# Optimization experiments

Hardware: AMD Instinct MI355X
Metric: run time of the kernel (lower is better)

Reference implementation:

```python
import jax, jax.numpy as jnp
import numpy as np

NUM_HEADS = 4
NUM_GROUPS = 8
EPS = 1e-5


def group_norm(x, gamma, beta):
    B, C, H, W = x.shape
    xg = x.reshape(B, NUM_GROUPS, C // NUM_GROUPS, H, W)
    mean = xg.mean(axis=(2, 3, 4), keepdims=True)
    var = xg.var(axis=(2, 3, 4), keepdims=True)
    xn = ((xg - mean) * jax.lax.rsqrt(var + EPS)).reshape(B, C, H, W)
    return xn * gamma[None, :, None, None] + beta[None, :, None, None]


def setup_inputs() -> dict:
    key = jax.random.key(0)
    k1, k2, k3 = jax.random.split(key, 3)
    B, C, H, W = 16, 512, 32, 32
    x = jax.random.normal(k1, (B, C, H, W), dtype=jnp.float32)
    gn_gamma = jnp.ones((C,), dtype=jnp.float32)
    gn_beta = jnp.zeros((C,), dtype=jnp.float32)
    w_qkv = jax.random.normal(k2, (3 * C, C), dtype=jnp.float32) * 0.02
    w_proj = jax.random.normal(k3, (C, C), dtype=jnp.float32) * 0.02
    b_proj = jnp.zeros((C,), dtype=jnp.float32)
    return {"x": x, "gn_gamma": gn_gamma, "gn_beta": gn_beta,
            "w_qkv": w_qkv, "w_proj": w_proj, "b_proj": b_proj}


def reference(x, gn_gamma, gn_beta, w_qkv, w_proj, b_proj):
    B, C, H, W = x.shape
    nh = NUM_HEADS
    hd = C // nh
    N = H * W

    x_norm = group_norm(x, gn_gamma, gn_beta)
    # 1x1 conv == channel matmul: (B,C,H,W) x (3C,C) -> (B,3C,H,W)
    qkv = jnp.einsum('bchw,dc->bdhw', x_norm, w_qkv)
    qkv = qkv.reshape(B, 3, nh, hd, N)
    q, k, v = qkv[:, 0], qkv[:, 1], qkv[:, 2]  # each (B, nh, hd, N)

    scale = hd ** (-0.5)
    attn = jnp.einsum('bhci,bhcj->bhij', q, k) * scale  # (B, nh, N, N)
    attn = jax.nn.softmax(attn, axis=-1)
    out = jnp.einsum('bhij,bhcj->bhci', attn, v)  # (B, nh, hd, N)
    out = out.reshape(B, C, H, W)

    proj = jnp.einsum('bchw,dc->bdhw', out, w_proj) + b_proj[None, :, None, None]
    return x + proj
```

## Files before the change

### kernel.cpp

```cpp
#include <hip/hip_runtime.h>
#include <stdint.h>

typedef unsigned char u8;
typedef unsigned short u16;
typedef unsigned int u32;
typedef long long i64;
typedef __attribute__((ext_vector_type(8))) short short8;
typedef __attribute__((ext_vector_type(4))) float f32x4;
typedef __attribute__((ext_vector_type(16))) float f32x16;
typedef __attribute__((ext_vector_type(4))) u32 u32x4;

#define BATCH 16
#define CCH   512
#define NPIX  1024
#define NGRP  8
#define CPG   64
#define NHEAD 4
#define HDIM  128

__device__ __forceinline__ u16 f2bf(float f) {
  union { float f; u32 u; } v; v.f = f;
  u32 u = v.u;
  u32 r = (u + 0x7FFFu + ((u >> 16) & 1u)) >> 16;
  return (u16)r;
}
__device__ __forceinline__ u8 f2fp8(float f) {
  return (u8)(__builtin_amdgcn_cvt_pk_fp8_f32(f, 0.f, 0, false) & 0xff);
}
__device__ __forceinline__ u32 pack4_fp8(float a, float b, float c, float d) {
  u32 w = (u32)__builtin_amdgcn_cvt_pk_fp8_f32(a, b, 0, false);
  w = (u32)__builtin_amdgcn_cvt_pk_fp8_f32(c, d, (int)w, true);
  return w;
}

__device__ __forceinline__ void gload16(const void* g, void* l) {
  typedef __attribute__((address_space(3))) u32 L;
  typedef __attribute__((address_space(1))) const u32 G;
  __builtin_amdgcn_global_load_lds((G*)(uintptr_t)g, (L*)(u32)(uintptr_t)l, 16, 0, 0);
}

#define PLSWAP(a, b) asm("v_permlane32_swap_b32 %0, %1" : "+v"(a), "+v"(b))

__device__ __forceinline__ short8 rd512(const char* base, int r, int ck, int hi) {
  int byte = ((r >> 2) * 512) +
             ((((r & 3) * 128) + ck * 32 + hi * 16) ^ (((r >> 2) & 15) << 4));
  return *reinterpret_cast<const short8*>(base + byte);
}

__global__ void gn_stats_k(const float* __restrict__ x, float* __restrict__ part) {
  int bg = blockIdx.x >> 3, sl = blockIdx.x & 7;
  const float* p = x + (size_t)bg * (CPG * NPIX) + sl * 8192;
  float s = 0.f, ss = 0.f;
  for (int i = threadIdx.x; i < 2048; i += 256) {
    float4 v = reinterpret_cast<const float4*>(p)[i];
    s  += v.x + v.y + v.z + v.w;
    ss += v.x*v.x + v.y*v.y + v.z*v.z + v.w*v.w;
  }
  for (int o = 32; o > 0; o >>= 1) { s += __shfl_down(s, o); ss += __shfl_down(ss, o); }
  __shared__ float sh[8];
  int wid = threadIdx.x >> 6;
  if ((threadIdx.x & 63) == 0) { sh[wid*2] = s; sh[wid*2+1] = ss; }
  __syncthreads();
  if (threadIdx.x == 0) {
    part[blockIdx.x*2]   = sh[0]+sh[2]+sh[4]+sh[6];
    part[blockIdx.x*2+1] = sh[1]+sh[3]+sh[5]+sh[7];
  }
}

__global__ __launch_bounds__(256) void gn_apply_t(const float* __restrict__ x,
                                                  const float* __restrict__ gamma,
                                                  const float* __restrict__ beta,
                                                  const float* __restrict__ part,
                                                  u16* __restrict__ xnT) {
  const int p0 = blockIdx.x * 64;
  const int c0 = blockIdx.y * 64;
  const int b  = blockIdx.z;
  __shared__ float lt[64][66];

  const int bg = b * NGRP + (c0 >> 6);
  float s = 0.f, ss = 0.f;
  #pragma unroll
  for (int k2 = 0; k2 < 8; ++k2) { s += part[(bg*8 + k2)*2]; ss += part[(bg*8 + k2)*2 + 1]; }
  const float invn = 1.f / (float)(CPG * NPIX);
  const float mean = s * invn;
  const float rstd = rsqrtf(ss * invn - mean * mean + 1e-5f);

  const int t = threadIdx.x;
  #pragma unroll
  for (int pass = 0; pass < 4; ++pass) {
    int c   = c0 + (t >> 4) + pass * 16;
    int pix = p0 + (t & 15) * 4;
    float ga = gamma[c] * rstd;
    float be = beta[c] - mean * ga;
    float4 v = *reinterpret_cast<const float4*>(&x[((size_t)(b*CCH + c)) * NPIX + pix]);
    int pl = (t & 15) * 4, cl = (t >> 4) + pass * 16;
    lt[pl+0][cl] = v.x*ga + be;
    lt[pl+1][cl] = v.y*ga + be;
    lt[pl+2][cl] = v.z*ga + be;
    lt[pl+3][cl] = v.w*ga + be;
  }
  __syncthreads();
  const int pl = t >> 2, cq = (t & 3) * 16;
  u32 wbuf[8];
  #pragma unroll
  for (int e = 0; e < 8; ++e) {
    u16 lo = f2bf(lt[pl][cq + e*2]);
    u16 hi = f2bf(lt[pl][cq + e*2 + 1]);
    wbuf[e] = (u32)lo | ((u32)hi << 16);
  }
  u32* dst = (u32*)&xnT[((size_t)(b*NPIX + p0 + pl)) * CCH + c0 + cq];
  #pragma unroll
  for (int e = 0; e < 8; ++e) dst[e] = wbuf[e];
}

__global__ void f2bf_all(const float* __restrict__ wqkv, const float* __restrict__ wproj,
                         u16* __restrict__ wq, u16* __restrict__ wp) {
  int i = blockIdx.x * 256 + threadIdx.x;
  float4 v; u16* dst;
  if (i < 196608) {
    v = reinterpret_cast<const float4*>(wqkv)[i];
    dst = wq + (size_t)i * 4;
  } else {
    v = reinterpret_cast<const float4*>(wproj)[i - 196608];
    dst = wp + (size_t)(i - 196608) * 4;
  }
  u32 lo = (u32)f2bf(v.x) | ((u32)f2bf(v.y) << 16);
  u32 hi = (u32)f2bf(v.z) | ((u32)f2bf(v.w) << 16);
  *reinterpret_cast<uint2*>(dst) = make_uint2(lo, hi);
}

__global__ __launch_bounds__(256, 2) void gemm_qkv(const u16* __restrict__ xnT,
                                                   const u16* __restrict__ wq_bf,
                                                   u8* __restrict__ outQ,
                                                   u8* __restrict__ outK,
                                                   u8* __restrict__ outV) {
  __shared__ __align__(16) char smem[65536];

  const int id = blockIdx.x;
  const int wg = (id & 7) * 192 + (id >> 3);
  const bool mode0 = (wg < 1024);
  int rt, ct;
  if (mode0) { rt = wg >> 3; ct = wg & 7; }
  else       { int w1 = wg - 1024; rt = w1 & 3; ct = w1 >> 2; }

  const char* Ab = mode0 ? (const char*)xnT + (size_t)rt * 131072
                         : (const char*)wq_bf + (size_t)(8 + rt) * 131072;
  const char* Bb = mode0 ? (const char*)wq_bf + (size_t)ct * 131072
                         : (const char*)xnT + (size_t)ct * 131072;

  const int t = threadIdx.x;
  const int lane = t & 63, w = t >> 6;
  const int q = lane & 31, hi = lane >> 5;
  const int rh = (w >> 1) * 64, ch = (w & 1) * 64;

  int soff[4];
  #pragma unroll
  for (int i = 0; i < 4; ++i) {
    int p = w*4096 + i*1024 + lane*16;
    int lrow = p >> 9, off = p & 511;
    int loff = off ^ ((lrow & 15) << 4);
    soff[i] = (lrow*4 + (loff >> 7)) * 1024 + (loff & 127);
  }

  #pragma unroll
  for (int i = 0; i < 4; ++i) {
    gload16(Ab + soff[i], smem +         w*4096 + i*1024);
    gload16(Bb + soff[i], smem + 16384 + w*4096 + i*1024);
  }

  f32x16 acc[2][2] = {};

  for (int kt = 0; kt < 8; ++kt) {
    asm volatile("s_waitcnt vmcnt(0)" ::: "memory");
    __syncthreads();
    const char* cur = smem + (kt & 1) * 32768;
    if (kt + 1 < 8) {
      char* nxt = smem + ((kt + 1) & 1) * 32768;
      #pragma unroll
      for (int i = 0; i < 4; ++i) {
        gload16(Ab + (kt+1)*128 + soff[i], nxt +         w*4096 + i*1024);
        gload16(Bb + (kt+1)*128 + soff[i], nxt + 16384 + w*4096 + i*1024);
      }
    }
    __builtin_amdgcn_s_setprio(1);
    #pragma unroll
    for (int ck = 0; ck < 4; ++ck) {
      short8 af0 = rd512(cur,         rh + q,      ck, hi);
      short8 af1 = rd512(cur,         rh + 32 + q, ck, hi);
      short8 bf0 = rd512(cur + 16384, ch + q,      ck, hi);
      short8 bf1 = rd512(cur + 16384, ch + 32 + q, ck, hi);
      acc[0][0] = __builtin_amdgcn_mfma_f32_32x32x16_bf16(af0, bf0, acc[0][0], 0, 0, 0);
      acc[0][1] = __builtin_amdgcn_mfma_f32_32x32x16_bf16(af0, bf1, acc[0][1], 0, 0, 0);
      acc[1][0] = __builtin_amdgcn_mfma_f32_32x32x16_bf16(af1, bf0, acc[1][0], 0, 0, 0);
      acc[1][1] = __builtin_amdgcn_mfma_f32_32x32x16_bf16(af1, bf1, acc[1][1], 0, 0, 0);
    }
    __builtin_amdgcn_s_setprio(0);
  }

  __syncthreads();
  u8* Dt = (u8*)smem;
  #pragma unroll
  for (int r = 0; r < 16; ++r) {
    int ar = (r & 3) + 8*(r >> 2) + 4*hi;
    Dt[(rh +      ar) * 144 + ch +      q] = f2fp8(acc[0][0][r]);
    Dt[(rh +      ar) * 144 + ch + 32 + q] = f2fp8(acc[0][1][r]);
    Dt[(rh + 32 + ar) * 144 + ch +      q] = f2fp8(acc[1][0][r]);
    Dt[(rh + 32 + ar) * 144 + ch + 32 + q] = f2fp8(acc[1][1][r]);
  }
  __syncthreads();

  const int rl = t >> 1, hoff = (t & 1) * 64;
  uint4 buf[4];
  const uint4* s4 = reinterpret_cast<const uint4*>(&Dt[rl*144 + hoff]);
  #pragma unroll
  for (int e = 0; e < 4; ++e) buf[e] = s4[e];

  u8* gdst;
  if (mode0) {
    const int tok0 = rt * 128;
    const int b = tok0 >> 10, pix0 = tok0 & 1023;
    const int h = ct & 3;
    u8* base = (ct >= 4) ? outK : outQ;
    gdst = base + ((size_t)((b*NHEAD + h)) * NPIX + pix0 + rl) * HDIM + hoff;
  } else {
    const int m0 = rt * 128, tok0 = ct * 128;
    const int b = tok0 >> 10, pix0 = tok0 & 1023;
    gdst = outV + ((size_t)(b*CCH + m0 + rl)) * NPIX + pix0 + hoff;
  }
  uint4* g4 = reinterpret_cast<uint4*>(gdst);
  #pragma unroll
  for (int e = 0; e < 4; ++e) g4[e] = buf[e];
}

__global__ __launch_bounds__(256, 2) void gemm_proj(const u16* __restrict__ wp_bf,
                                                    const u16* __restrict__ attnO,
                                                    const float* __restrict__ xres,
                                                    const float* __restrict__ bias,
                                                    float* __restrict__ outF) {
  __shared__ __align__(16) char smem[65536];

  const int id = blockIdx.x;
  const int wg = (id & 7) * 64 + (id >> 3);
  const int rt = wg & 3, ct = wg >> 2;

  const char* Ab = (const char*)wp_bf + (size_t)rt * 131072;
  const char* Bb = (const char*)attnO + (size_t)ct * 131072;

  const int t = threadIdx.x;
  const int lane = t & 63, w = t >> 6;
  const int q = lane & 31, hi = lane >> 5;
  const int rh = (w >> 1) * 64, ch = (w & 1) * 64;

  int soff[4];
  #pragma unroll
  for (int i = 0; i < 4; ++i) {
    int p = w*4096 + i*1024 + lane*16;
    int lrow = p >> 9, off = p & 511;
    int loff = off ^ ((lrow & 15) << 4);
    soff[i] = (lrow*4 + (loff >> 7)) * 1024 + (loff & 127);
  }

  #pragma unroll
  for (int i = 0; i < 4; ++i) {
    gload16(Ab + soff[i], smem +         w*4096 + i*1024);
    gload16(Bb + soff[i], smem + 16384 + w*4096 + i*1024);
  }

  f32x16 acc[2][2] = {};

  for (int kt = 0; kt < 8; ++kt) {
    asm volatile("s_waitcnt vmcnt(0)" ::: "memory");
    __syncthreads();
    const char* cur = smem + (kt & 1) * 32768;
    if (kt + 1 < 8) {
      char* nxt = smem + ((kt + 1) & 1) * 32768;
      #pragma unroll
      for (int i = 0; i < 4; ++i) {
        gload16(Ab + (kt+1)*128 + soff[i], nxt +         w*4096 + i*1024);
        gload16(Bb + (kt+1)*128 + soff[i], nxt + 16384 + w*4096 + i*1024);
      }
    }
    __builtin_amdgcn_s_setprio(1);
    #pragma unroll
    for (int ck = 0; ck < 4; ++ck) {
      short8 af0 = rd512(cur,         rh + q,      ck, hi);
      short8 af1 = rd512(cur,         rh + 32 + q, ck, hi);
      short8 bf0 = rd512(cur + 16384, ch + q,      ck, hi);
      short8 bf1 = rd512(cur + 16384, ch + 32 + q, ck, hi);
      acc[0][0] = __builtin_amdgcn_mfma_f32_32x32x16_bf16(af0, bf0, acc[0][0], 0, 0, 0);
      acc[0][1] = __builtin_amdgcn_mfma_f32_32x32x16_bf16(af0, bf1, acc[0][1], 0, 0, 0);
      acc[1][0] = __builtin_amdgcn_mfma_f32_32x32x16_bf16(af1, bf0, acc[1][0], 0, 0, 0);
      acc[1][1] = __builtin_amdgcn_mfma_f32_32x32x16_bf16(af1, bf1, acc[1][1], 0, 0, 0);
    }
    __builtin_amdgcn_s_setprio(0);
  }

  const int m0 = rt * 128, tok0 = ct * 128;
  const int b = tok0 >> 10, pix0 = tok0 & 1023;
  #pragma unroll
  for (int r = 0; r < 16; ++r) {
    int ar = (r & 3) + 8*(r >> 2) + 4*hi;
    int m0r = m0 + rh + ar, m1r = m0 + rh + 32 + ar;
    size_t o00 = ((size_t)(b*CCH + m0r)) * NPIX + pix0 + ch + q;
    size_t o01 = o00 + 32;
    size_t o10 = ((size_t)(b*CCH + m1r)) * NPIX + pix0 + ch + q;
    size_t o11 = o10 + 32;
    outF[o00] = xres[o00] + acc[0][0][r] + bias[m0r];
    outF[o01] = xres[o01] + acc[0][1][r] + bias[m0r];
    outF[o10] = xres[o10] + acc[1][0][r] + bias[m1r];
    outF[o11] = xres[o11] + acc[1][1][r] + bias[m1r];
  }
}

__global__ __launch_bounds__(256, 2) void attn_k(const u8* __restrict__ Qt,
                                                 const u8* __restrict__ Kt,
                                                 const u8* __restrict__ Vb,
                                                 u16* __restrict__ attnO) {
  int id = blockIdx.x;
  int swz = (id & 7) * 64 + (id >> 3);
  const int qt = swz & 7;
  const int h  = (swz >> 3) & 3;
  const int b  = swz >> 5;
  const int bh = b * NHEAD + h;

  __shared__ __align__(16) char smem[32768];

  const int t = threadIdx.x;
  const int lane = t & 63, w = t >> 6;
  const int q = lane & 31, hi = lane >> 5;

  const u8*   Qb    = Qt + ((size_t)bh * NPIX + qt*128 + w*32 + q) * HDIM;
  const char* Kbase = (const char*)Kt + (size_t)bh * NPIX * HDIM;
  const char* Vbase = (const char*)Vb + ((size_t)b*CCH + h*HDIM) * NPIX;

  i64 qf[8];
  #pragma unroll
  for (int ck = 0; ck < 8; ++ck)
    qf[ck] = *reinterpret_cast<const i64*>(Qb + ck*16 + hi*8);

  int koff[2], voff[2];
  #pragma unroll
  for (int i = 0; i < 2; ++i) {
    int d = i*4096 + w*1024 + lane*16;
    int r = d >> 7, x = d & 127;
    koff[i] = r*128 + (x ^ ((r & 15) << 3));
    int vc = 2*r + (x >> 6);
    voff[i] = vc*1024 + ((x & 63) ^ ((r & 7) << 3));
  }

  const int ksw = (q & 15) << 3;

  f32x16 of[4] = {};
  float l_run = 0.f;
  i64 pf[4];
  const float qs2 = 0.08838834764831845f * 1.44269504088896f;

  #pragma unroll
  for (int i = 0; i < 2; ++i)
    gload16(Kbase + koff[i],        smem +        i*4096 + w*1024);
  #pragma unroll
  for (int i = 0; i < 2; ++i)
    gload16(Kbase + 8192 + koff[i], smem + 8192 + i*4096 + w*1024);
  #pragma unroll
  for (int i = 0; i < 2; ++i)
    gload16(Vbase + voff[i],        smem + 16384 + i*4096 + w*1024);
  asm volatile("s_waitcnt vmcnt(0)" ::: "memory");
  __syncthreads();

  {
    f32x16 sn0 = {}, sn1 = {};
    #pragma unroll
    for (int ck = 0; ck < 8; ++ck) {
      const i64 kf0 = *reinterpret_cast<const i64*>(smem + q*128      + ((ck*16 + hi*8) ^ ksw));
      const i64 kf1 = *reinterpret_cast<const i64*>(smem + (32+q)*128 + ((ck*16 + hi*8) ^ ksw));
      sn0 = __builtin_amdgcn_mfma_f32_32x32x16_fp8_fp8(kf0, qf[ck], sn0, 0, 0, 0);
      sn1 = __builtin_amdgcn_mfma_f32_32x32x16_fp8_fp8(kf1, qf[ck], sn1, 0, 0, 0);
    }
    float ps = 0.f;
    float p[16];
    #pragma unroll
    for (int g = 0; g < 2; ++g) {
      const f32x16& sn = g ? sn1 : sn0;
      #pragma unroll
      for (int r = 0; r < 16; ++r) { p[r] = exp2f(sn[r] * qs2); ps += p[r]; }
      u32 pkl0 = pack4_fp8(p[0], p[1], p[2], p[3]);
      u32 pkh0 = pack4_fp8(p[4], p[5], p[6], p[7]);
      u32 pkl1 = pack4_fp8(p[8], p[9], p[10], p[11]);
      u32 pkh1 = pack4_fp8(p[12], p[13], p[14], p[15]);
      PLSWAP(pkl0, pkh0);
      PLSWAP(pkl1, pkh1);
      pf[g*2]   = (i64)(((unsigned long long)pkh0 << 32) | pkl0);
      pf[g*2+1] = (i64)(((unsigned long long)pkh1 << 32) | pkl1);
    }
    ps += __shfl_xor(ps, 32);
    l_run += ps;
  }

  for (int tt = 0; tt < 16; ++tt) {
    asm volatile("s_waitcnt vmcnt(2)" ::: "memory");
    __builtin_amdgcn_s_barrier();

    const char* kcur = smem + (((tt+1) & 1) << 13);
    const char* vcur = smem + 16384 + ((tt & 1) << 13);

    if (tt + 2 < 16) {
      char* kd = smem + ((tt & 1) << 13);
      #pragma unroll
      for (int i = 0; i < 2; ++i)
        gload16(Kbase + (size_t)(tt+2)*8192 + koff[i], kd + i*4096 + w*1024);
    }
    if (tt + 1 < 16) {
      char* vd = smem + 16384 + (((tt+1) & 1) << 13);
      #pragma unroll
      for (int i = 0; i < 2; ++i)
        gload16(Vbase + (size_t)(tt+1)*64 + voff[i], vd + i*4096 + w*1024);
    }

    f32x16 sn0 = {}, sn1 = {};
    __builtin_amdgcn_s_setprio(1);
    if (tt + 1 < 16) {
      #pragma unroll
      for (int ck = 0; ck < 8; ++ck) {
        const i64 kf0 = *reinterpret_cast<const i64*>(kcur + q*128      + ((ck*16 + hi*8) ^ ksw));
        const i64 kf1 = *reinterpret_cast<const i64*>(kcur + (32+q)*128 + ((ck*16 + hi*8) ^ ksw));
        sn0 = __builtin_amdgcn_mfma_f32_32x32x16_fp8_fp8(kf0, qf[ck], sn0, 0, 0, 0);
        sn1 = __builtin_amdgcn_mfma_f32_32x32x16_fp8_fp8(kf1, qf[ck], sn1, 0, 0, 0);
      }
    }
    __builtin_amdgcn_s_setprio(0);

    if (tt < 14)       asm volatile("s_waitcnt vmcnt(4)" ::: "memory");
    else if (tt == 14) asm volatile("s_waitcnt vmcnt(2)" ::: "memory");
    else               asm volatile("s_waitcnt vmcnt(0)" ::: "memory");
    __builtin_amdgcn_s_barrier();

    __builtin_amdgcn_s_setprio(1);
    #pragma unroll
    for (int cg = 0; cg < 4; ++cg) {
      const int c = cg*32 + q;
      const char* vrow = vcur + (c >> 1)*128 + (c & 1)*64;
      const int vsw = ((c >> 1) & 7) << 3;
      #pragma unroll
      for (int kc = 0; kc < 4; ++kc) {
        const i64 vf = *reinterpret_cast<const i64*>(vrow + ((kc*16 + hi*8) ^ vsw));
        of[cg] = __builtin_amdgcn_mfma_f32_32x32x16_fp8_fp8(vf, pf[kc], of[cg], 0, 0, 0);
      }
    }
    __builtin_amdgcn_s_setprio(0);

    if (tt + 1 < 16) {
      float ps = 0.f;
      float p[16];
      #pragma unroll
      for (int g = 0; g < 2; ++g) {
        const f32x16& sn = g ? sn1 : sn0;
        #pragma unroll
        for (int r = 0; r < 16; ++r) { p[r] = exp2f(sn[r] * qs2); ps += p[r]; }
        u32 pkl0 = pack4_fp8(p[0], p[1], p[2], p[3]);
        u32 pkh0 = pack4_fp8(p[4], p[5], p[6], p[7]);
        u32 pkl1 = pack4_fp8(p[8], p[9], p[10], p[11]);
        u32 pkh1 = pack4_fp8(p[12], p[13], p[14], p[15]);
        PLSWAP(pkl0, pkh0);
        PLSWAP(pkl1, pkh1);
        pf[g*2]   = (i64)(((unsigned long long)pkh0 << 32) | pkl0);
        pf[g*2+1] = (i64)(((unsigned long long)pkh1 << 32) | pkl1);
      }
      ps += __shfl_xor(ps, 32);
      l_run += ps;
    }
  }

  float inv = 1.f / l_run;
  u16* orow = attnO + ((size_t)(b*NPIX + qt*128 + w*32 + q)) * CCH + h*HDIM;
  #pragma unroll
  for (int cg = 0; cg < 4; ++cg) {
    #pragma unroll
    for (int u = 0; u < 8; ++u) {
      int c = cg*32 + ((2*u) & 3) + 8*(u >> 1) + 4*hi;
      u32 pk = (u32)f2bf(of[cg][2*u] * inv) | ((u32)f2bf(of[cg][2*u+1] * inv) << 16);
      *reinterpret_cast<u32*>(&orow[c]) = pk;
    }
  }
}

extern "C" void kernel_launch(void* const* d_in, const int* in_sizes, int n_in,
                              void* d_out, int out_size, void* d_ws, size_t ws_size,
                              hipStream_t stream) {
  const float* x     = (const float*)d_in[0];
  const float* gamma = (const float*)d_in[1];
  const float* beta  = (const float*)d_in[2];
  const float* wqkv  = (const float*)d_in[3];
  const float* wproj = (const float*)d_in[4];
  const float* bproj = (const float*)d_in[5];
  float* out = (float*)d_out;

  char* ws = (char*)d_ws;
  float* part   = (float*)ws;
  u16*   xnT    = (u16*)(ws + 8192);
  u16*   wq_bf  = (u16*)(ws + 8192 + (16u<<20));
  u16*   wp_bf  = (u16*)((char*)wq_bf + 1572864);
  u8*    Qt     = (u8*)((char*)wp_bf + 524288);
  u8*    Kt     = (u8*)((char*)Qt + (8u<<20));
  u8*    Vb     = (u8*)((char*)Kt + (8u<<20));
  u16*   attnO  = (u16*)((char*)Vb + (8u<<20));

  gn_stats_k<<<dim3(1024), dim3(256), 0, stream>>>(x, part);
  gn_apply_t<<<dim3(16, 8, BATCH), dim3(256), 0, stream>>>(x, gamma, beta, part, xnT);
  f2bf_all<<<dim3(1024), dim3(256), 0, stream>>>(wqkv, wproj, wq_bf, wp_bf);

  gemm_qkv<<<dim3(1536), dim3(256), 0, stream>>>(xnT, wq_bf, Qt, Kt, Vb);

  attn_k<<<dim3(512), dim3(256), 0, stream>>>(Qt, Kt, Vb, attnO);

  gemm_proj<<<dim3(512), dim3(256), 0, stream>>>(wp_bf, attnO, x, bproj, out);
}
```

Before: 113.0 us.

## Split attention KV tile across warp pairs with shared-memory reduction, double grid

Each attention block now covers 64 query rows instead of 128. The four warps form two query sub-tiles by two halves of every 64-key tile, so each warp runs half the QK and PV MFMAs per iteration. The two partial outputs and row sums are combined through shared memory at the end. This halves per-warp accumulator and P-fragment registers so launch bounds can request 4 blocks per SM, and it doubles the grid to 1024 blocks for more parallelism. The cost is loading each K/V tile into LDS twice as often across blocks, plus an extra reduction pass and barrier at the end.

```diff
diff --git a/kernel.cpp b/kernel.cpp
--- a/kernel.cpp
+++ b/kernel.cpp
@@ -8,7 +8,6 @@
 typedef __attribute__((ext_vector_type(8))) short short8;
 typedef __attribute__((ext_vector_type(4))) float f32x4;
 typedef __attribute__((ext_vector_type(16))) float f32x16;
-typedef __attribute__((ext_vector_type(4))) u32 u32x4;
 
 #define BATCH 16
 #define CCH   512
@@ -45,6 +44,28 @@
   int byte = ((r >> 2) * 512) +
              ((((r & 3) * 128) + ck * 32 + hi * 16) ^ (((r >> 2) & 15) << 4));
   return *reinterpret_cast<const short8*>(base + byte);
+}
+
+__device__ __forceinline__ float softmax_pack16(const f32x16& sn, float qs2, i64* pf) {
+  float p0, p1, p2, p3, ps;
+  u32 w0, w1, w2, w3;
+  p0 = exp2f(sn[0]*qs2);  p1 = exp2f(sn[1]*qs2);
+  p2 = exp2f(sn[2]*qs2);  p3 = exp2f(sn[3]*qs2);
+  ps = (p0+p1)+(p2+p3);  w0 = pack4_fp8(p0, p1, p2, p3);
+  p0 = exp2f(sn[4]*qs2);  p1 = exp2f(sn[5]*qs2);
+  p2 = exp2f(sn[6]*qs2);  p3 = exp2f(sn[7]*qs2);
+  ps += (p0+p1)+(p2+p3); w1 = pack4_fp8(p0, p1, p2, p3);
+  p0 = exp2f(sn[8]*qs2);  p1 = exp2f(sn[9]*qs2);
+  p2 = exp2f(sn[10]*qs2); p3 = exp2f(sn[11]*qs2);
+  ps += (p0+p1)+(p2+p3); w2 = pack4_fp8(p0, p1, p2, p3);
+  p0 = exp2f(sn[12]*qs2); p1 = exp2f(sn[13]*qs2);
+  p2 = exp2f(sn[14]*qs2); p3 = exp2f(sn[15]*qs2);
+  ps += (p0+p1)+(p2+p3); w3 = pack4_fp8(p0, p1, p2, p3);
+  PLSWAP(w0, w1);
+  PLSWAP(w2, w3);
+  pf[0] = (i64)(((unsigned long long)w1 << 32) | w0);
+  pf[1] = (i64)(((unsigned long long)w3 << 32) | w2);
+  return ps;
 }
 
 __global__ void gn_stats_k(const float* __restrict__ x, float* __restrict__ part) {
@@ -312,24 +333,25 @@
   }
 }
 
-__global__ __launch_bounds__(256, 2) void attn_k(const u8* __restrict__ Qt,
+__global__ __launch_bounds__(256, 4) void attn_k(const u8* __restrict__ Qt,
                                                  const u8* __restrict__ Kt,
                                                  const u8* __restrict__ Vb,
                                                  u16* __restrict__ attnO) {
   int id = blockIdx.x;
-  int swz = (id & 7) * 64 + (id >> 3);
-  const int qt = swz & 7;
-  const int h  = (swz >> 3) & 3;
-  const int b  = swz >> 5;
+  int swz = (id & 7) * 128 + (id >> 3);
+  const int qt = swz & 15;
+  const int h  = (swz >> 4) & 3;
+  const int b  = swz >> 6;
   const int bh = b * NHEAD + h;
 
-  __shared__ __align__(16) char smem[32768];
+  __shared__ __align__(16) char smem[33024];
 
   const int t = threadIdx.x;
   const int lane = t & 63, w = t >> 6;
   const int q = lane & 31, hi = lane >> 5;
-
-  const u8*   Qb    = Qt + ((size_t)bh * NPIX + qt*128 + w*32 + q) * HDIM;
+  const int qsub = w & 1, kvh = w >> 1;
+
+  const u8*   Qb    = Qt + ((size_t)bh * NPIX + qt*64 + qsub*32 + q) * HDIM;
   const char* Kbase = (const char*)Kt + (size_t)bh * NPIX * HDIM;
   const char* Vbase = (const char*)Vb + ((size_t)b*CCH + h*HDIM) * NPIX;
 
@@ -348,11 +370,13 @@
     voff[i] = vc*1024 + ((x & 63) ^ ((r & 7) << 3));
   }
 
-  const int ksw = (q & 15) << 3;
+  const int ksw  = (q & 15) << 3;
+  const int krow = (kvh*32 + q) * 128;
+  const int vkv  = kvh * 32;
 
   f32x16 of[4] = {};
   float l_run = 0.f;
-  i64 pf[4];
+  i64 pf[2];
   const float qs2 = 0.08838834764831845f * 1.44269504088896f;
 
   #pragma unroll
@@ -368,32 +392,13 @@
   __syncthreads();
 
   {
-    f32x16 sn0 = {}, sn1 = {};
+    f32x16 sn = {};
     #pragma unroll
     for (int ck = 0; ck < 8; ++ck) {
-      const i64 kf0 = *reinterpret_cast<const i64*>(smem + q*128      + ((ck*16 + hi*8) ^ ksw));
-      const i64 kf1 = *reinterpret_cast<const i64*>(smem + (32+q)*128 + ((ck*16 + hi*8) ^ ksw));
-      sn0 = __builtin_amdgcn_mfma_f32_32x32x16_fp8_fp8(kf0, qf[ck], sn0, 0, 0, 0);
-      sn1 = __builtin_amdgcn_mfma_f32_32x32x16_fp8_fp8(kf1, qf[ck], sn1, 0, 0, 0);
-    }
-    float ps = 0.f;
-    float p[16];
-    #pragma unroll
-    for (int g = 0; g < 2; ++g) {
-      const f32x16& sn = g ? sn1 : sn0;
-      #pragma unroll
-      for (int r = 0; r < 16; ++r) { p[r] = exp2f(sn[r] * qs2); ps += p[r]; }
-      u32 pkl0 = pack4_fp8(p[0], p[1], p[2], p[3]);
-      u32 pkh0 = pack4_fp8(p[4], p[5], p[6], p[7]);
-      u32 pkl1 = pack4_fp8(p[8], p[9], p[10], p[11]);
-      u32 pkh1 = pack4_fp8(p[12], p[13], p[14], p[15]);
-      PLSWAP(pkl0, pkh0);
-      PLSWAP(pkl1, pkh1);
-      pf[g*2]   = (i64)(((unsigned long long)pkh0 << 32) | pkl0);
-      pf[g*2+1] = (i64)(((unsigned long long)pkh1 << 32) | pkl1);
-    }
-    ps += __shfl_xor(ps, 32);
-    l_run += ps;
+      const i64 kf = *reinterpret_cast<const i64*>(smem + krow + ((ck*16 + hi*8) ^ ksw));
+      sn = __builtin_amdgcn_mfma_f32_32x32x16_fp8_fp8(kf, qf[ck], sn, 0, 0, 0);
+    }
+    l_run += softmax_pack16(sn, qs2, pf);
   }
 
   for (int tt = 0; tt < 16; ++tt) {
@@ -416,15 +421,13 @@
         gload16(Vbase + (size_t)(tt+1)*64 + voff[i], vd + i*4096 + w*1024);
     }
 
-    f32x16 sn0 = {}, sn1 = {};
+    f32x16 sn = {};
     __builtin_amdgcn_s_setprio(1);
     if (tt + 1 < 16) {
       #pragma unroll
       for (int ck = 0; ck < 8; ++ck) {
-        const i64 kf0 = *reinterpret_cast<const i64*>(kcur + q*128      + ((ck*16 + hi*8) ^ ksw));
-        const i64 kf1 = *reinterpret_cast<const i64*>(kcur + (32+q)*128 + ((ck*16 + hi*8) ^ ksw));
-        sn0 = __builtin_amdgcn_mfma_f32_32x32x16_fp8_fp8(kf0, qf[ck], sn0, 0, 0, 0);
-        sn1 = __builtin_amdgcn_mfma_f32_32x32x16_fp8_fp8(kf1, qf[ck], sn1, 0, 0, 0);
+        const i64 kf = *reinterpret_cast<const i64*>(kcur + krow + ((ck*16 + hi*8) ^ ksw));
+        sn = __builtin_amdgcn_mfma_f32_32x32x16_fp8_fp8(kf, qf[ck], sn, 0, 0, 0);
       }
     }
     __builtin_amdgcn_s_setprio(0);
@@ -441,44 +444,43 @@
       const char* vrow = vcur + (c >> 1)*128 + (c & 1)*64;
       const int vsw = ((c >> 1) & 7) << 3;
       #pragma unroll
-      for (int kc = 0; kc < 4; ++kc) {
-        const i64 vf = *reinterpret_cast<const i64*>(vrow + ((kc*16 + hi*8) ^ vsw));
+      for (int kc = 0; kc < 2; ++kc) {
+        const i64 vf = *reinterpret_cast<const i64*>(vrow + ((vkv + kc*16 + hi*8) ^ vsw));
         of[cg] = __builtin_amdgcn_mfma_f32_32x32x16_fp8_fp8(vf, pf[kc], of[cg], 0, 0, 0);
       }
     }
     __builtin_amdgcn_s_setprio(0);
 
-    if (tt + 1 < 16) {
-      float ps = 0.f;
-      float p[16];
-      #pragma unroll
-      for (int g = 0; g < 2; ++g) {
-        const f32x16& sn = g ? sn1 : sn0;
-        #pragma unroll
-        for (int r = 0; r < 16; ++r) { p[r] = exp2f(sn[r] * qs2); ps += p[r]; }
-        u32 pkl0 = pack4_fp8(p[0], p[1], p[2], p[3]);
-        u32 pkh0 = pack4_fp8(p[4], p[5], p[6], p[7]);
-        u32 pkl1 = pack4_fp8(p[8], p[9], p[10], p[11]);
-        u32 pkh1 = pack4_fp8(p[12], p[13], p[14], p[15]);
-        PLSWAP(pkl0, pkh0);
-        PLSWAP(pkl1, pkh1);
-        pf[g*2]   = (i64)(((unsigned long long)pkh0 << 32) | pkl0);
-        pf[g*2+1] = (i64)(((unsigned long long)pkh1 << 32) | pkl1);
+    if (tt + 1 < 16)
+      l_run += softmax_pack16(sn, qs2, pf);
+  }
+
+  l_run += __shfl_xor(l_run, 32);
+  __syncthreads();
+  float* exf = (float*)smem;
+  float* exl = (float*)(smem + 32768);
+
+  if (kvh == 1) {
+    #pragma unroll
+    for (int cg = 0; cg < 4; ++cg)
+      #pragma unroll
+      for (int r = 0; r < 16; ++r)
+        exf[qsub*4096 + cg*1024 + r*64 + lane] = of[cg][r];
+    if (lane < 32) exl[qsub*32 + q] = l_run;
+  }
+  __syncthreads();
+  if (kvh == 0) {
+    const float inv = 1.f / (l_run + exl[qsub*32 + q]);
+    u16* orow = attnO + ((size_t)(b*NPIX + qt*64 + qsub*32 + q)) * CCH + h*HDIM;
+    #pragma unroll
+    for (int cg = 0; cg < 4; ++cg) {
+      #pragma unroll
+      for (int u = 0; u < 8; ++u) {
+        int c = cg*32 + ((2*u) & 3) + 8*(u >> 1) + 4*hi;
+        float a0 = (of[cg][2*u]   + exf[qsub*4096 + cg*1024 + (2*u)*64   + lane]) * inv;
+        float a1 = (of[cg][2*u+1] + exf[qsub*4096 + cg*1024 + (2*u+1)*64 + lane]) * inv;
+        *reinterpret_cast<u32*>(&orow[c]) = (u32)f2bf(a0) | ((u32)f2bf(a1) << 16);
       }
-      ps += __shfl_xor(ps, 32);
-      l_run += ps;
-    }
-  }
-
-  float inv = 1.f / l_run;
-  u16* orow = attnO + ((size_t)(b*NPIX + qt*128 + w*32 + q)) * CCH + h*HDIM;
-  #pragma unroll
-  for (int cg = 0; cg < 4; ++cg) {
-    #pragma unroll
-    for (int u = 0; u < 8; ++u) {
-      int c = cg*32 + ((2*u) & 3) + 8*(u >> 1) + 4*hi;
-      u32 pk = (u32)f2bf(of[cg][2*u] * inv) | ((u32)f2bf(of[cg][2*u+1] * inv) << 16);
-      *reinterpret_cast<u32*>(&orow[c]) = pk;
     }
   }
 }
@@ -510,7 +512,7 @@
 
   gemm_qkv<<<dim3(1536), dim3(256), 0, stream>>>(xnT, wq_bf, Qt, Kt, Vb);
 
-  attn_k<<<dim3(512), dim3(256), 0, stream>>>(Qt, Kt, Vb, attnO);
+  attn_k<<<dim3(1024), dim3(256), 0, stream>>>(Qt, Kt, Vb, attnO);
 
   gemm_proj<<<dim3(512), dim3(256), 0, stream>>>(wp_bf, attnO, x, bproj, out);
 }
```

After: 121.6 us. 7.6% more time.
